# Kernel optimization log

Hardware: AMD Instinct MI355X
Metric: run time of the kernel (lower is better)

Reference implementation:

```python
import jax, jax.numpy as jnp
import numpy as np

DIM = 1024
HEADS = 16
SCALE = DIM ** (-0.5)  # note: full dim, matching original module


def setup_inputs() -> dict:
    key = jax.random.key(0)
    k1, k2, k3, k4 = jax.random.split(key, 4)
    x = jax.random.normal(k1, (8, 1024, DIM), dtype=jnp.float32)
    w_qkv = jax.random.normal(k2, (DIM, 3 * DIM), dtype=jnp.float32) * (DIM ** -0.5)
    w_out = jax.random.normal(k3, (DIM, DIM), dtype=jnp.float32) * (DIM ** -0.5)
    b_out = jax.random.normal(k4, (DIM,), dtype=jnp.float32) * 0.01
    return {"x": x, "w_qkv": w_qkv, "w_out": w_out, "b_out": b_out}


def reference(x, w_qkv, w_out, b_out):
    b, n, dim = x.shape
    h = HEADS
    d = dim // h
    qkv = x @ w_qkv  # [b, n, 3*dim]
    q, k, v = jnp.split(qkv, 3, axis=-1)
    # 'b n (h d) -> b h n d'
    def to_heads(t):
        return t.reshape(b, n, h, d).transpose(0, 2, 1, 3)
    q, k, v = to_heads(q), to_heads(k), to_heads(v)
    dots = jnp.einsum('bhid,bhjd->bhij', q, k) * SCALE
    attn = jax.nn.softmax(dots, axis=-1)
    out = jnp.einsum('bhij,bhjd->bhid', attn, v)
    out = out.transpose(0, 2, 1, 3).reshape(b, n, dim)  # 'b h n d -> b n (h d)'
    return out @ w_out + b_out  # dropout is identity (rate=0 / eval)
```

## Files before the change

kernel.cpp:

```cpp
#include <hip/hip_runtime.h>

typedef __bf16 bf16x8 __attribute__((ext_vector_type(8)));
typedef __bf16 bf16x4 __attribute__((ext_vector_type(4)));
typedef float  f32x4  __attribute__((ext_vector_type(4)));

#define MFMA16(a, b, c) __builtin_amdgcn_mfma_f32_16x16x32_bf16(a, b, c, 0, 0, 0)
#define GLL(gp, lp) __builtin_amdgcn_global_load_lds( \
    (__attribute__((address_space(1))) void*)(gp),    \
    (__attribute__((address_space(3))) void*)(lp), 16, 0, 0)
#define WAITBAR(N) asm volatile("s_waitcnt vmcnt(" #N ") lgkmcnt(0)\n\ts_barrier" ::: "memory")

__global__ __launch_bounds__(256) void cast_x_kernel(const float* __restrict__ in,
                                                     __bf16* __restrict__ out) {
  int i = blockIdx.x * 256 + threadIdx.x;
  const float4 v = ((const float4*)in)[i];
  bf16x4 o = {(__bf16)v.x, (__bf16)v.y, (__bf16)v.z, (__bf16)v.w};
  ((bf16x4*)out)[i] = o;
}

__global__ void transpose_cast_kernel(const float* __restrict__ in,
                                      __bf16* __restrict__ out,
                                      int rows, int cols) {
  __shared__ float tile[32][33];
  int tx = threadIdx.x, ty = threadIdx.y;
  int x = blockIdx.x * 32 + tx;
  int y0 = blockIdx.y * 32;
#pragma unroll
  for (int i = 0; i < 32; i += 8)
    tile[ty + i][tx] = in[(y0 + ty + i) * cols + x];
  __syncthreads();
  int ox = y0 + tx;
  int oy0 = blockIdx.x * 32;
#pragma unroll
  for (int i = 0; i < 32; i += 8)
    out[(oy0 + ty + i) * rows + ox] = (__bf16)tile[tx][ty + i];
}

#define QSCALE 0.045084220027780106f
__global__ __launch_bounds__(256) void gemm_bt_kernel(
    const __bf16* __restrict__ A, const __bf16* __restrict__ Bt, int mode, int nxg,
    __bf16* __restrict__ qo, __bf16* __restrict__ ko, __bf16* __restrict__ vo,
    float* __restrict__ outp, const float* __restrict__ bias) {
  __shared__ __bf16 LDS[3][2][4096];
  const int tid = threadIdx.x;
  const int id = blockIdx.x;
  const int xcd = id & 7, s = id >> 3;
  const int bx = xcd * nxg + (nxg == 3 ? s % 3 : 0);
  const int by = (nxg == 3 ? s / 3 : s);
  const int m0 = by * 128, n0 = bx * 128;
  const int w = tid >> 6, lane = tid & 63;
  const int quad = lane >> 4, l15 = lane & 15;
  const int wm = (w >> 1) * 64, wn = (w & 1) * 64;
  f32x4 acc[4][4] = {};
  const int sr = tid >> 2;
  const int sc = (tid & 3) * 8;
  const __bf16* ag = A + (m0 + sr) * 1024 + sc;
  const __bf16* bg = Bt + (n0 + sr) * 1024 + sc;

  auto stage = [&](int T, int b) {
    const int kk = T * 32;
    GLL(ag + kk,             &LDS[b][0][0] + w * 512);
    GLL(ag + 64 * 1024 + kk, &LDS[b][0][0] + 2048 + w * 512);
    GLL(bg + kk,             &LDS[b][1][0] + w * 512);
    GLL(bg + 64 * 1024 + kk, &LDS[b][1][0] + 2048 + w * 512);
  };
  auto compute = [&](int b) {
    const __bf16* Asb = &LDS[b][0][0];
    const __bf16* Bsb = &LDS[b][1][0];
    bf16x8 af[4], bfr[4];
#pragma unroll
    for (int i = 0; i < 4; ++i)
      af[i] = *(const bf16x8*)(Asb + (wm + i * 16 + l15) * 32 + quad * 8);
#pragma unroll
    for (int j = 0; j < 4; ++j)
      bfr[j] = *(const bf16x8*)(Bsb + (wn + j * 16 + l15) * 32 + quad * 8);
#pragma unroll
    for (int i = 0; i < 4; ++i)
#pragma unroll
      for (int j = 0; j < 4; ++j)
        acc[i][j] = MFMA16(af[i], bfr[j], acc[i][j]);
  };

  stage(0, 0);
  stage(1, 1);
  WAITBAR(4);
  for (int g = 0; g < 10; ++g) {
    const int t = g * 3;
    stage(t + 2, 2); compute(0); WAITBAR(4);
    stage(t + 3, 0); compute(1); WAITBAR(4);
    stage(t + 4, 1); compute(2); WAITBAR(4);
  }
  compute(0);
  asm volatile("s_waitcnt vmcnt(0) lgkmcnt(0)\n\ts_barrier" ::: "memory");
  compute(1);
  __syncthreads();

  const int gcw = n0 + wn;
  float* T = (float*)(&LDS[0][0][0]) + w * 1088;
  if (mode == 0) {
    const int which = gcw >> 10;
    const int h = (gcw & 1023) >> 6;
    if (which == 2) {
#pragma unroll
      for (int i = 0; i < 4; ++i) {
        int gm = m0 + wm + i * 16 + quad * 4;
        int b = gm >> 10, n = gm & 1023;
        __bf16* vb = vo + ((long)(b * 16 + h) * 64) * 1024 + n;
#pragma unroll
        for (int j = 0; j < 4; ++j) {
          int dd = j * 16 + l15;
          bf16x4 pv = {(__bf16)acc[i][j][0], (__bf16)acc[i][j][1],
                       (__bf16)acc[i][j][2], (__bf16)acc[i][j][3]};
          *(bf16x4*)(vb + (long)dd * 1024) = pv;
        }
      }
    } else {
      __bf16* dst = (which == 0) ? qo : ko;
      const float scl = (which == 0) ? QSCALE : 1.0f;
#pragma unroll
      for (int i = 0; i < 4; ++i) {
#pragma unroll
        for (int j = 0; j < 4; ++j)
#pragma unroll
          for (int r = 0; r < 4; ++r)
            T[(quad * 4 + r) * 68 + j * 16 + l15] = acc[i][j][r];
        const float* Tr = T + l15 * 68 + quad * 16;
        f32x4 c0 = *(const f32x4*)(Tr);
        f32x4 c1 = *(const f32x4*)(Tr + 4);
        f32x4 c2 = *(const f32x4*)(Tr + 8);
        f32x4 c3 = *(const f32x4*)(Tr + 12);
        int gm = m0 + wm + i * 16 + l15;
        int b = gm >> 10, n = gm & 1023;
        __bf16* p = dst + ((long)((b * 16 + h) * 1024 + n)) * 64 + quad * 16;
        bf16x8 o0 = {(__bf16)(c0[0] * scl), (__bf16)(c0[1] * scl),
                     (__bf16)(c0[2] * scl), (__bf16)(c0[3] * scl),
                     (__bf16)(c1[0] * scl), (__bf16)(c1[1] * scl),
                     (__bf16)(c1[2] * scl), (__bf16)(c1[3] * scl)};
        bf16x8 o1 = {(__bf16)(c2[0] * scl), (__bf16)(c2[1] * scl),
                     (__bf16)(c2[2] * scl), (__bf16)(c2[3] * scl),
                     (__bf16)(c3[0] * scl), (__bf16)(c3[1] * scl),
                     (__bf16)(c3[2] * scl), (__bf16)(c3[3] * scl)};
        *(bf16x8*)p = o0;
        *(bf16x8*)(p + 8) = o1;
      }
    }
  } else {
    const int cb = gcw;
    f32x4 bv[4];
#pragma unroll
    for (int c = 0; c < 4; ++c)
      bv[c] = *(const f32x4*)(bias + cb + quad * 16 + c * 4);
#pragma unroll
    for (int i = 0; i < 4; ++i) {
#pragma unroll
      for (int j = 0; j < 4; ++j)
#pragma unroll
        for (int r = 0; r < 4; ++r)
          T[(quad * 4 + r) * 68 + j * 16 + l15] = acc[i][j][r];
      const float* Tr = T + l15 * 68 + quad * 16;
      int gm = m0 + wm + i * 16 + l15;
      float* p = outp + (long)gm * 1024 + cb + quad * 16;
#pragma unroll
      for (int c = 0; c < 4; ++c) {
        f32x4 v = *(const f32x4*)(Tr + c * 4);
        v += bv[c];
        *(f32x4*)(p + c * 4) = v;
      }
    }
  }
}

__global__ __launch_bounds__(256, 4) void attn_kernel(
    const __bf16* __restrict__ q, const __bf16* __restrict__ k,
    const __bf16* __restrict__ vt, __bf16* __restrict__ ao) {
  __shared__ __bf16 Ks[128 * 64];
  __shared__ __bf16 Vs[64 * 128];
  __shared__ __bf16 Ps[4][32 * 32];
  const int tid = threadIdx.x;
  const int bh = blockIdx.x & 127, qt = blockIdx.x >> 7;
  const int w = tid >> 6, lane = tid & 63;
  const int quad = lane >> 4, l15 = lane & 15;
  const int qrow = qt * 128 + w * 32;
  const __bf16* qb = q + (bh * 1024 + qrow) * 64;
  bf16x8 qf[2][2];
#pragma unroll
  for (int f = 0; f < 2; ++f) {
    qf[f][0] = *(const bf16x8*)(qb + (f * 16 + l15) * 64 + quad * 8);
    qf[f][1] = *(const bf16x8*)(qb + (f * 16 + l15) * 64 + 32 + quad * 8);
  }
  f32x4 o[2][4] = {};
  float rs0 = 0.f, rs1 = 0.f;
  const int krow = tid >> 3, kg8 = tid & 7;
  const __bf16* kg = k + (bh * 1024 + krow) * 64 + kg8 * 8;
  const int ksw = ((kg8 ^ (krow & 7)) * 8);
  const int vrow = tid >> 2, vg4 = tid & 3;
  const __bf16* vg = vt + (bh * 64 + vrow) * 1024 + vg4 * 8;
  const int kfs0 = (quad ^ (l15 & 7)) * 8;
  const int kfs1 = ((4 + quad) ^ (l15 & 7)) * 8;
  __bf16* pw = Ps[w];
  const int psw = quad ^ (l15 & 3);
  for (int j0 = 0; j0 < 1024; j0 += 128) {
    bf16x8 kv[4], vv[4];
#pragma unroll
    for (int p = 0; p < 4; ++p) kv[p] = *(const bf16x8*)(kg + (j0 + p * 32) * 64);
#pragma unroll
    for (int p = 0; p < 4; ++p) vv[p] = *(const bf16x8*)(vg + j0 + p * 32);
    __syncthreads();
#pragma unroll
    for (int p = 0; p < 4; ++p)
      *(bf16x8*)(Ks + (krow + p * 32) * 64 + ksw) = kv[p];
#pragma unroll
    for (int p = 0; p < 4; ++p)
      *(bf16x8*)(Vs + vrow * 128 + (((p * 4 + vg4) ^ (vrow & 15)) * 8)) = vv[p];
    __syncthreads();
    bf16x4 pk[2][8];
#pragma unroll
    for (int t = 0; t < 8; ++t) {
      const __bf16* kr = Ks + (t * 16 + l15) * 64;
      bf16x8 kf0 = *(const bf16x8*)(kr + kfs0);
      bf16x8 kf1 = *(const bf16x8*)(kr + kfs1);
      f32x4 z0 = {}, z1 = {};
      z0 = MFMA16(kf0, qf[0][0], z0);
      z0 = MFMA16(kf1, qf[0][1], z0);
      z1 = MFMA16(kf0, qf[1][0], z1);
      z1 = MFMA16(kf1, qf[1][1], z1);
      float p00 = exp2f(z0[0]), p01 = exp2f(z0[1]), p02 = exp2f(z0[2]), p03 = exp2f(z0[3]);
      float p10 = exp2f(z1[0]), p11 = exp2f(z1[1]), p12 = exp2f(z1[2]), p13 = exp2f(z1[3]);
      rs0 += (p00 + p01) + (p02 + p03);
      rs1 += (p10 + p11) + (p12 + p13);
      pk[0][t] = (bf16x4){(__bf16)p00, (__bf16)p01, (__bf16)p02, (__bf16)p03};
      pk[1][t] = (bf16x4){(__bf16)p10, (__bf16)p11, (__bf16)p12, (__bf16)p13};
    }
#pragma unroll
    for (int Q = 0; Q < 4; ++Q) {
#pragma unroll
      for (int f = 0; f < 2; ++f)
#pragma unroll
        for (int tl = 0; tl < 2; ++tl) {
          int g = (2 * tl + (quad >> 1)) ^ (l15 & 3);
          *(bf16x4*)(pw + (f * 16 + l15) * 32 + g * 8 + (quad & 1) * 4) = pk[f][2 * Q + tl];
        }
      bf16x8 pf0 = *(const bf16x8*)(pw + l15 * 32 + psw * 8);
      bf16x8 pf1 = *(const bf16x8*)(pw + (16 + l15) * 32 + psw * 8);
#pragma unroll
      for (int dt = 0; dt < 4; ++dt) {
        bf16x8 vf = *(const bf16x8*)(Vs + (dt * 16 + l15) * 128 + (((Q * 4 + quad) ^ l15) * 8));
        o[0][dt] = MFMA16(pf0, vf, o[0][dt]);
        o[1][dt] = MFMA16(pf1, vf, o[1][dt]);
      }
    }
  }
  rs0 += __shfl_xor(rs0, 16); rs0 += __shfl_xor(rs0, 32);
  rs1 += __shfl_xor(rs1, 16); rs1 += __shfl_xor(rs1, 32);
  const int b = bh >> 4, h = bh & 15;
  const int qbase = quad << 4;
#pragma unroll
  for (int r = 0; r < 4; ++r) {
    int src = qbase | (quad * 4 + r);
    float inv0 = 1.0f / __shfl(rs0, src);
    float inv1 = 1.0f / __shfl(rs1, src);
    long row0 = b * 1024 + qrow + quad * 4 + r;
    long row1 = row0 + 16;
#pragma unroll
    for (int dt = 0; dt < 4; ++dt) {
      ao[row0 * 1024 + h * 64 + dt * 16 + l15] = (__bf16)(o[0][dt][r] * inv0);
      ao[row1 * 1024 + h * 64 + dt * 16 + l15] = (__bf16)(o[1][dt][r] * inv1);
    }
  }
}

extern "C" void kernel_launch(void* const* d_in, const int* in_sizes, int n_in,
                              void* d_out, int out_size, void* d_ws, size_t ws_size,
                              hipStream_t stream) {
  const float* x = (const float*)d_in[0];
  const float* w_qkv = (const float*)d_in[1];
  const float* w_out = (const float*)d_in[2];
  const float* b_out = (const float*)d_in[3];
  float* out = (float*)d_out;

  char* ws = (char*)d_ws;
  __bf16* xb    = (__bf16*)(ws);
  __bf16* wqkvt = (__bf16*)(ws + 16777216);
  __bf16* woutt = (__bf16*)(ws + 23068672);
  __bf16* qw    = (__bf16*)(ws + 25165824);
  __bf16* kw    = (__bf16*)(ws + 41943040);
  __bf16* vw    = (__bf16*)(ws + 58720256);
  __bf16* ao    = xb;

  cast_x_kernel<<<8192, 256, 0, stream>>>(x, xb);
  transpose_cast_kernel<<<dim3(96, 32), dim3(32, 8), 0, stream>>>(w_qkv, wqkvt, 1024, 3072);
  transpose_cast_kernel<<<dim3(32, 32), dim3(32, 8), 0, stream>>>(w_out, woutt, 1024, 1024);
  gemm_bt_kernel<<<1536, 256, 0, stream>>>(xb, wqkvt, 0, 3, qw, kw, vw, nullptr, nullptr);
  attn_kernel<<<1024, 256, 0, stream>>>(qw, kw, vw, ao);
  gemm_bt_kernel<<<512, 256, 0, stream>>>(ao, woutt, 1, 1, nullptr, nullptr, nullptr, out, b_out);
}
```

Measured before the change: 276.0 us.

## Enlarge attention query tile to 64 rows per wave and prefetch next K/V tile

Each wave now handles 64 query rows instead of 32, so every K/V tile staged in LDS is reused by twice as many rows, and the grid is halved to 512 blocks. The next K/V chunk is loaded from global memory into registers while the current one is being computed, overlapping load latency with MFMA work. The P staging buffer becomes padded (stride 40) instead of XOR-swizzled, and the score computation is interleaved per Q sub-block. In exchange, register pressure rises (launch bounds drop to 2 blocks/CU) and fewer blocks are available to fill the GPU.

```diff
diff --git a/kernel.cpp b/kernel.cpp
--- a/kernel.cpp
+++ b/kernel.cpp
@@ -170,41 +170,40 @@
   }
 }
 
-__global__ __launch_bounds__(256, 4) void attn_kernel(
+__global__ __launch_bounds__(256, 2) void attn_kernel(
     const __bf16* __restrict__ q, const __bf16* __restrict__ k,
     const __bf16* __restrict__ vt, __bf16* __restrict__ ao) {
   __shared__ __bf16 Ks[128 * 64];
   __shared__ __bf16 Vs[64 * 128];
-  __shared__ __bf16 Ps[4][32 * 32];
+  __shared__ __bf16 Ps[4][64 * 40];
   const int tid = threadIdx.x;
   const int bh = blockIdx.x & 127, qt = blockIdx.x >> 7;
   const int w = tid >> 6, lane = tid & 63;
   const int quad = lane >> 4, l15 = lane & 15;
-  const int qrow = qt * 128 + w * 32;
-  const __bf16* qb = q + (bh * 1024 + qrow) * 64;
-  bf16x8 qf[2][2];
-#pragma unroll
-  for (int f = 0; f < 2; ++f) {
-    qf[f][0] = *(const bf16x8*)(qb + (f * 16 + l15) * 64 + quad * 8);
-    qf[f][1] = *(const bf16x8*)(qb + (f * 16 + l15) * 64 + 32 + quad * 8);
-  }
-  f32x4 o[2][4] = {};
-  float rs0 = 0.f, rs1 = 0.f;
+  const int qrow = qt * 256 + w * 64;
+  bf16x8 qf[4][2];
+#pragma unroll
+  for (int f = 0; f < 4; ++f) {
+    const __bf16* qb = q + ((long)(bh * 1024 + qrow + f * 16 + l15)) * 64;
+    qf[f][0] = *(const bf16x8*)(qb + quad * 8);
+    qf[f][1] = *(const bf16x8*)(qb + 32 + quad * 8);
+  }
+  f32x4 o[4][4] = {};
+  float rs[4] = {0.f, 0.f, 0.f, 0.f};
   const int krow = tid >> 3, kg8 = tid & 7;
   const __bf16* kg = k + (bh * 1024 + krow) * 64 + kg8 * 8;
-  const int ksw = ((kg8 ^ (krow & 7)) * 8);
+  const int ksw = (kg8 ^ (krow & 7)) * 8;
   const int vrow = tid >> 2, vg4 = tid & 3;
   const __bf16* vg = vt + (bh * 64 + vrow) * 1024 + vg4 * 8;
   const int kfs0 = (quad ^ (l15 & 7)) * 8;
   const int kfs1 = ((4 + quad) ^ (l15 & 7)) * 8;
   __bf16* pw = Ps[w];
-  const int psw = quad ^ (l15 & 3);
+  bf16x8 kv[4], vv[4];
+#pragma unroll
+  for (int p = 0; p < 4; ++p) kv[p] = *(const bf16x8*)(kg + (p * 32) * 64);
+#pragma unroll
+  for (int p = 0; p < 4; ++p) vv[p] = *(const bf16x8*)(vg + p * 32);
   for (int j0 = 0; j0 < 1024; j0 += 128) {
-    bf16x8 kv[4], vv[4];
-#pragma unroll
-    for (int p = 0; p < 4; ++p) kv[p] = *(const bf16x8*)(kg + (j0 + p * 32) * 64);
-#pragma unroll
-    for (int p = 0; p < 4; ++p) vv[p] = *(const bf16x8*)(vg + j0 + p * 32);
     __syncthreads();
 #pragma unroll
     for (int p = 0; p < 4; ++p)
@@ -213,60 +212,62 @@
     for (int p = 0; p < 4; ++p)
       *(bf16x8*)(Vs + vrow * 128 + (((p * 4 + vg4) ^ (vrow & 15)) * 8)) = vv[p];
     __syncthreads();
-    bf16x4 pk[2][8];
-#pragma unroll
-    for (int t = 0; t < 8; ++t) {
-      const __bf16* kr = Ks + (t * 16 + l15) * 64;
-      bf16x8 kf0 = *(const bf16x8*)(kr + kfs0);
-      bf16x8 kf1 = *(const bf16x8*)(kr + kfs1);
-      f32x4 z0 = {}, z1 = {};
-      z0 = MFMA16(kf0, qf[0][0], z0);
-      z0 = MFMA16(kf1, qf[0][1], z0);
-      z1 = MFMA16(kf0, qf[1][0], z1);
-      z1 = MFMA16(kf1, qf[1][1], z1);
-      float p00 = exp2f(z0[0]), p01 = exp2f(z0[1]), p02 = exp2f(z0[2]), p03 = exp2f(z0[3]);
-      float p10 = exp2f(z1[0]), p11 = exp2f(z1[1]), p12 = exp2f(z1[2]), p13 = exp2f(z1[3]);
-      rs0 += (p00 + p01) + (p02 + p03);
-      rs1 += (p10 + p11) + (p12 + p13);
-      pk[0][t] = (bf16x4){(__bf16)p00, (__bf16)p01, (__bf16)p02, (__bf16)p03};
-      pk[1][t] = (bf16x4){(__bf16)p10, (__bf16)p11, (__bf16)p12, (__bf16)p13};
+    if (j0 + 128 < 1024) {
+#pragma unroll
+      for (int p = 0; p < 4; ++p) kv[p] = *(const bf16x8*)(kg + (j0 + 128 + p * 32) * 64);
+#pragma unroll
+      for (int p = 0; p < 4; ++p) vv[p] = *(const bf16x8*)(vg + j0 + 128 + p * 32);
     }
 #pragma unroll
     for (int Q = 0; Q < 4; ++Q) {
 #pragma unroll
-      for (int f = 0; f < 2; ++f)
-#pragma unroll
-        for (int tl = 0; tl < 2; ++tl) {
-          int g = (2 * tl + (quad >> 1)) ^ (l15 & 3);
-          *(bf16x4*)(pw + (f * 16 + l15) * 32 + g * 8 + (quad & 1) * 4) = pk[f][2 * Q + tl];
+      for (int tl = 0; tl < 2; ++tl) {
+        const int t = 2 * Q + tl;
+        const __bf16* kr = Ks + (t * 16 + l15) * 64;
+        bf16x8 kf0 = *(const bf16x8*)(kr + kfs0);
+        bf16x8 kf1 = *(const bf16x8*)(kr + kfs1);
+#pragma unroll
+        for (int f = 0; f < 4; ++f) {
+          f32x4 z = {};
+          z = MFMA16(kf0, qf[f][0], z);
+          z = MFMA16(kf1, qf[f][1], z);
+          float p0 = exp2f(z[0]), p1 = exp2f(z[1]), p2 = exp2f(z[2]), p3 = exp2f(z[3]);
+          rs[f] += (p0 + p1) + (p2 + p3);
+          *(bf16x4*)(pw + (f * 16 + l15) * 40 + tl * 16 + quad * 4) =
+              (bf16x4){(__bf16)p0, (__bf16)p1, (__bf16)p2, (__bf16)p3};
         }
-      bf16x8 pf0 = *(const bf16x8*)(pw + l15 * 32 + psw * 8);
-      bf16x8 pf1 = *(const bf16x8*)(pw + (16 + l15) * 32 + psw * 8);
+      }
+      bf16x8 pf[4];
+#pragma unroll
+      for (int f = 0; f < 4; ++f)
+        pf[f] = *(const bf16x8*)(pw + (f * 16 + l15) * 40 + quad * 8);
 #pragma unroll
       for (int dt = 0; dt < 4; ++dt) {
         bf16x8 vf = *(const bf16x8*)(Vs + (dt * 16 + l15) * 128 + (((Q * 4 + quad) ^ l15) * 8));
-        o[0][dt] = MFMA16(pf0, vf, o[0][dt]);
-        o[1][dt] = MFMA16(pf1, vf, o[1][dt]);
-      }
-    }
-  }
-  rs0 += __shfl_xor(rs0, 16); rs0 += __shfl_xor(rs0, 32);
-  rs1 += __shfl_xor(rs1, 16); rs1 += __shfl_xor(rs1, 32);
+#pragma unroll
+        for (int f = 0; f < 4; ++f)
+          o[f][dt] = MFMA16(pf[f], vf, o[f][dt]);
+      }
+    }
+  }
+#pragma unroll
+  for (int f = 0; f < 4; ++f) {
+    rs[f] += __shfl_xor(rs[f], 16);
+    rs[f] += __shfl_xor(rs[f], 32);
+  }
   const int b = bh >> 4, h = bh & 15;
   const int qbase = quad << 4;
 #pragma unroll
-  for (int r = 0; r < 4; ++r) {
-    int src = qbase | (quad * 4 + r);
-    float inv0 = 1.0f / __shfl(rs0, src);
-    float inv1 = 1.0f / __shfl(rs1, src);
-    long row0 = b * 1024 + qrow + quad * 4 + r;
-    long row1 = row0 + 16;
-#pragma unroll
-    for (int dt = 0; dt < 4; ++dt) {
-      ao[row0 * 1024 + h * 64 + dt * 16 + l15] = (__bf16)(o[0][dt][r] * inv0);
-      ao[row1 * 1024 + h * 64 + dt * 16 + l15] = (__bf16)(o[1][dt][r] * inv1);
-    }
-  }
+  for (int f = 0; f < 4; ++f)
+#pragma unroll
+    for (int r = 0; r < 4; ++r) {
+      int src = qbase | (quad * 4 + r);
+      float inv = 1.0f / __shfl(rs[f], src);
+      long row = b * 1024 + qrow + f * 16 + quad * 4 + r;
+#pragma unroll
+      for (int dt = 0; dt < 4; ++dt)
+        ao[row * 1024 + h * 64 + dt * 16 + l15] = (__bf16)(o[f][dt][r] * inv);
+    }
 }
 
 extern "C" void kernel_launch(void* const* d_in, const int* in_sizes, int n_in,
@@ -291,6 +292,6 @@
   transpose_cast_kernel<<<dim3(96, 32), dim3(32, 8), 0, stream>>>(w_qkv, wqkvt, 1024, 3072);
   transpose_cast_kernel<<<dim3(32, 32), dim3(32, 8), 0, stream>>>(w_out, woutt, 1024, 1024);
   gemm_bt_kernel<<<1536, 256, 0, stream>>>(xb, wqkvt, 0, 3, qw, kw, vw, nullptr, nullptr);
-  attn_kernel<<<1024, 256, 0, stream>>>(qw, kw, vw, ao);
+  attn_kernel<<<512, 256, 0, stream>>>(qw, kw, vw, ao);
   gemm_bt_kernel<<<512, 256, 0, stream>>>(ao, woutt, 1, 1, nullptr, nullptr, nullptr, out, b_out);
 }
```

New measurement: 278.4 us. About the same (+0.9%).
